# Kernel optimization log

Hardware: AMD Instinct MI355X
Metric: run time of the kernel (lower is better)

## Reference

```python
import jax, jax.numpy as jnp
import numpy as np

D1 = 4096
D2 = 4096
K = 838860  # int(D1*D2*0.05)
ALPHA = 16.0


def setup_inputs() -> dict:
    key = jax.random.key(0)
    k1, k2, k3, k4, k5 = jax.random.split(key, 5)
    x = jax.random.normal(k1, (2, 64, D1), jnp.float32)
    W_base = jax.random.normal(k2, (D2, D1), jnp.float32) * 0.02  # torch Linear weight (out, in)
    b_base = jnp.zeros((D2,), jnp.float32)
    c_re = jax.random.normal(k3, (K,), jnp.float32) * 0.02
    c_im = jax.random.normal(k4, (K,), jnp.float32) * 0.02
    # unique flat positions of the top-k frequency coefficients (stand-in for topk of |fft2(delta_W_init)|)
    mask_idx = jax.random.permutation(k5, D1 * D2)[:K].astype(jnp.int32)
    return {"x": x, "W_base": W_base, "b_base": b_base,
            "c_re": c_re, "c_im": c_im, "mask_idx": mask_idx}


def reference(x, W_base, b_base, c_re, c_im, mask_idx):
    # scatter sparse complex coefficients into dense frequency matrix
    c = (c_re + 1j * c_im).astype(jnp.complex64)
    F_flat = jnp.zeros((D1 * D2,), jnp.complex64).at[mask_idx].set(c)
    # inverse 2D FFT -> real part -> scale by alpha
    Delta_W = jnp.fft.ifft2(F_flat.reshape(D1, D2)).real.astype(jnp.float32) * ALPHA  # [D1, D2]
    # frozen base linear: h = x @ W_base.T + b
    h = jnp.einsum('bnd,fd->bnf', x, W_base) + b_base
    # LoRA-style low-frequency update
    return h + jnp.einsum('bnd,df->bnf', x, Delta_W)
```

## Files before the change

### kernel.cpp

```cpp
#include <hip/hip_runtime.h>


#define TWO_PI 6.28318530717958647692f
constexpr int NROW = 128;
constexpr float SCALE_A = 16.0f / 16777216.0f;
constexpr int NCHUNK = 256;
constexpr int KC = 4;

typedef unsigned short ushort_t;
using short8 = __attribute__((ext_vector_type(8))) short;
using f32x4  = __attribute__((ext_vector_type(4))) float;

__device__ __forceinline__ ushort_t f2bf(float f) {
  unsigned u = __float_as_uint(f);
  u = (u + 0x7FFFu + ((u >> 16) & 1u)) >> 16;
  return (ushort_t)u;
}
__device__ __forceinline__ unsigned cvtpk(float lo, float hi) {
  unsigned r;
  asm("v_cvt_pk_bf16_f32 %0, %1, %2" : "=v"(r) : "v"(lo), "v"(hi));
  return r;
}
__device__ __forceinline__ float bflo(unsigned u) { return __int_as_float((int)(u << 16)); }
__device__ __forceinline__ float bfhi(unsigned u) { return __int_as_float((int)(u & 0xffff0000u)); }
__device__ __forceinline__ void dot2(float& acc, unsigned a, unsigned b) {
  asm("v_dot2_f32_bf16 %0, %1, %2, %0" : "+v"(acc) : "v"(a), "v"(b));
}
__device__ __forceinline__ void dot2s(float& acc, unsigned a, unsigned b) {
  asm("v_dot2_f32_bf16 %0, %1, %2, %0" : "+v"(acc) : "s"(a), "v"(b));
}
__device__ __forceinline__ void gload_lds16(const void* g, void* l) {
  __builtin_amdgcn_global_load_lds(
      (const __attribute__((address_space(1))) unsigned*)g,
      (__attribute__((address_space(3))) unsigned*)l, 16, 0, 0);
}

__global__ __launch_bounds__(1024) void fused_stage1(const float* __restrict__ x,
                                                     unsigned* __restrict__ XTb,
                                                     const int* __restrict__ idx, int K,
                                                     int chunk, int* __restrict__ cnt,
                                                     ushort_t* __restrict__ xbf) {
  __shared__ __align__(16) char smem[25600];
  const int bx = blockIdx.x, tid = threadIdx.x;
  if (bx >= 512) {
    int i = (bx - 512) * 1024 + tid;
    float4 v = ((const float4*)x)[i];
    ((uint2*)xbf)[i] = make_uint2(cvtpk(v.x, v.y), cvtpk(v.z, v.w));
    return;
  }
  if (bx < 256) {
    float*    xs   = (float*)smem;
    unsigned* bp   = (unsigned*)(smem + 16384);
    float2*   w64f = (float2*)(smem + 24576);
    unsigned* wA   = (unsigned*)(smem + 25088);
    unsigned* wB   = (unsigned*)(smem + 25344);
    const int t = bx & 127, qi = bx >> 7;
    const float* xrow = x + (size_t)t * 4096;
#pragma unroll
    for (int l = 0; l < 4; ++l) xs[tid + 1024 * l] = xrow[tid + 1024 * l];
    if (tid < 64) {
      float s, c; __sincosf(TWO_PI * (float)tid * (1.0f / 64.0f), &s, &c);
      w64f[tid] = make_float2(c, s);
      wA[tid] = cvtpk(c, -s);
      wB[tid] = cvtpk(s, c);
    }
    __syncthreads();
#pragma unroll
    for (int l = 0; l < 2; ++l) {
      int o = tid + 1024 * l, m1 = o >> 5, k1l = o & 31, k1 = qi * 32 + k1l;
      float ar = 0.f, ai = 0.f;
      for (int m2 = 0; m2 < 64; ++m2) {
        float xv = xs[m1 + (m2 << 6)];
        float2 w = w64f[(m2 * k1) & 63];
        ar = fmaf(xv, w.x, ar); ai = fmaf(xv, w.y, ai);
      }
      float s, c; __sincosf((float)(m1 * k1) * (TWO_PI / 4096.0f), &s, &c);
      bp[(m1 << 5) + k1l] = cvtpk(ar * c - ai * s, ar * s + ai * c);
    }
    __syncthreads();
    {
      const int k1l = tid & 31, k2 = tid >> 5;
      const int k = qi * 32 + k1l + (k2 << 6);
      float xr = 0.f, xi = 0.f;
      for (int m1 = 0; m1 < 64; ++m1) {
        unsigned wi = (unsigned)((m1 * k2) & 63);
        unsigned bv = bp[(m1 << 5) + k1l];
        dot2(xr, wA[wi], bv);
        dot2(xi, wB[wi], bv);
      }
      XTb[(size_t)k * NROW + t] = cvtpk(xr, xi);
      if (qi == 0 && tid == 0) {
        float xr2 = 0.f, xi2 = 0.f;
        for (int m1 = 0; m1 < 64; ++m1) {
          float sgn = (m1 & 1) ? -1.f : 1.f;
          unsigned bv = bp[m1 << 5];
          xr2 = fmaf(sgn, bflo(bv), xr2);
          xi2 = fmaf(sgn, bfhi(bv), xi2);
        }
        XTb[(size_t)2048 * NROW + t] = cvtpk(xr2, xi2);
      }
    }
  } else {
    int* h = (int*)smem;
    const int c = bx - 256;
#pragma unroll
    for (int l = 0; l < 4; ++l) h[tid + 1024 * l] = 0;
    __syncthreads();
    const int j0 = c * chunk, j1 = min(j0 + chunk, K);
    for (int j = j0 + tid; j < j1; j += 1024) atomicAdd(&h[idx[j] & 4095], 1);
    __syncthreads();
#pragma unroll
    for (int l = 0; l < 4; ++l) cnt[(size_t)c * 4096 + tid + 1024 * l] = h[tid + 1024 * l];
  }
}

__global__ __launch_bounds__(256) void colscan(int* __restrict__ cnt, int* __restrict__ tot) {
  const int k2 = blockIdx.x * 256 + threadIdx.x;
  int run = 0;
  for (int c16 = 0; c16 < NCHUNK; c16 += 16) {
    int v[16];
#pragma unroll
    for (int i = 0; i < 16; ++i) v[i] = cnt[(size_t)(c16 + i) * 4096 + k2];
#pragma unroll
    for (int i = 0; i < 16; ++i) {
      cnt[(size_t)(c16 + i) * 4096 + k2] = run;
      run += v[i];
    }
  }
  tot[k2] = run;
}

__global__ __launch_bounds__(1024) void scan4096(const int* __restrict__ count,
                                                 int* __restrict__ off) {
  __shared__ int s[4096];
  int tid = threadIdx.x;
#pragma unroll
  for (int l = 0; l < 4; ++l) s[tid + 1024 * l] = count[tid + 1024 * l];
  __syncthreads();
  for (int d = 1; d < 4096; d <<= 1) {
    int v[4];
#pragma unroll
    for (int l = 0; l < 4; ++l) {
      int i = tid + 1024 * l;
      v[l] = s[i] + ((i >= d) ? s[i - d] : 0);
    }
    __syncthreads();
#pragma unroll
    for (int l = 0; l < 4; ++l) s[tid + 1024 * l] = v[l];
    __syncthreads();
  }
#pragma unroll
  for (int l = 0; l < 4; ++l) {
    int i = tid + 1024 * l;
    off[i] = s[i] - count[i];
  }
}

__global__ __launch_bounds__(1024) void scatter2(const int* __restrict__ idx,
                                                 const float* __restrict__ cre,
                                                 const float* __restrict__ cim, int K,
                                                 int chunk, const int* __restrict__ base,
                                                 const int* __restrict__ off,
                                                 uint2* __restrict__ bucket) {
  __shared__ int lbase[4096];
  __shared__ int lcur[4096];
  const int c = blockIdx.x, tid = threadIdx.x;
#pragma unroll
  for (int l = 0; l < 4; ++l) {
    int k2 = tid + 1024 * l;
    lbase[k2] = base[(size_t)c * 4096 + k2] + off[k2];
    lcur[k2] = 0;
  }
  __syncthreads();
  const int j0 = c * chunk, j1 = min(j0 + chunk, K);
  for (int j = j0 + tid; j < j1; j += 1024) {
    int p = idx[j];
    int k2 = p & 4095;
    int r = atomicAdd(&lcur[k2], 1);
    unsigned cr = f2bf(cre[j]), ci = f2bf(cim[j]);
    bucket[lbase[k2] + r] = make_uint2((unsigned)(p >> 12) | (cr << 16), ci << 16);
  }
}

#define SP_ISS1(g, u, AP, BP, XV) { \
    unsigned w0_ = (unsigned)__builtin_amdgcn_readlane((int)ec.x, (g) * 8 + (u)); \
    unsigned w1_ = (unsigned)__builtin_amdgcn_readlane((int)ec.y, (g) * 8 + (u)); \
    int k1_ = (int)(w0_ & 0xfffu); \
    unsigned cj_ = (k1_ > 2048) ? 0x8000u : 0u; \
    int r_ = (k1_ > 2048) ? 4096 - k1_ : k1_; \
    AP[u] = (w0_ >> 16) | ((((w1_ >> 16) ^ 0x8000u ^ cj_)) << 16); \
    BP[u] = (w1_ >> 16) | ((((w0_ >> 16) ^ cj_)) << 16); \
    const unsigned* p_ = XTb + (size_t)r_ * NROW; \
    asm volatile("global_load_dwordx2 %0, %1, %2" \
                 : "=v"(XV) : "v"(voff), "s"(p_) : "memory"); }
#define SP_ISS8(g, AP, BP, X) \
    SP_ISS1(g, 0, AP, BP, X##0) SP_ISS1(g, 1, AP, BP, X##1) \
    SP_ISS1(g, 2, AP, BP, X##2) SP_ISS1(g, 3, AP, BP, X##3) \
    SP_ISS1(g, 4, AP, BP, X##4) SP_ISS1(g, 5, AP, BP, X##5) \
    SP_ISS1(g, 6, AP, BP, X##6) SP_ISS1(g, 7, AP, BP, X##7)
#define SP_WAIT8(X) \
    asm volatile("s_waitcnt vmcnt(8)" \
                 : "+v"(X##0), "+v"(X##1), "+v"(X##2), "+v"(X##3), \
                   "+v"(X##4), "+v"(X##5), "+v"(X##6), "+v"(X##7) :: "memory"); \
    __builtin_amdgcn_sched_barrier(0);
#define SP_WAIT0(X) \
    asm volatile("s_waitcnt vmcnt(0)" \
                 : "+v"(X##0), "+v"(X##1), "+v"(X##2), "+v"(X##3), \
                   "+v"(X##4), "+v"(X##5), "+v"(X##6), "+v"(X##7) :: "memory"); \
    __builtin_amdgcn_sched_barrier(0);
#define SP_CMP1(u, AP, BP, XV) \
    dot2s(ar0, AP[u], XV.x); dot2s(ai0, BP[u], XV.x); \
    dot2s(ar1, AP[u], XV.y); dot2s(ai1, BP[u], XV.y);
#define SP_CMP8(AP, BP, X) \
    SP_CMP1(0, AP, BP, X##0) SP_CMP1(1, AP, BP, X##1) \
    SP_CMP1(2, AP, BP, X##2) SP_CMP1(3, AP, BP, X##3) \
    SP_CMP1(4, AP, BP, X##4) SP_CMP1(5, AP, BP, X##5) \
    SP_CMP1(6, AP, BP, X##6) SP_CMP1(7, AP, BP, X##7)

__global__ __launch_bounds__(256, 4) void fused_heavy(const uint2* __restrict__ bucket,
                                                      const int* __restrict__ off,
                                                      const int* __restrict__ count,
                                                      const unsigned* __restrict__ XTb,
                                                      unsigned* __restrict__ Yp,
                                                      const ushort_t* __restrict__ xbf,
                                                      const float* __restrict__ W,
                                                      ushort_t* __restrict__ partb) {
  __shared__ __align__(16) char smem[16384];
  const int tid = threadIdx.x;
  const int w = tid >> 6, lane = tid & 63;
  if (blockIdx.x >= 256) {
    float4* red = (float4*)smem;
    const int colsel = w >> 1, half = w & 1;
    const int k2 = (blockIdx.x - 256) * 2 + colsel;
    const int s = off[k2], n = count[k2];
    const unsigned voff = lane * 8;
    float ar0 = 0.f, ai0 = 0.f, ar1 = 0.f, ai1 = 0.f;
    for (int c = half * 64; c < n; c += 128) {
      int idx = c + lane;
      uint2 ec = (idx < n) ? bucket[s + idx] : make_uint2(0u, 0u);
      unsigned ApA[8], BpA[8], ApB[8], BpB[8];
      uint2 xa0, xa1, xa2, xa3, xa4, xa5, xa6, xa7;
      uint2 xb0, xb1, xb2, xb3, xb4, xb5, xb6, xb7;
      SP_ISS8(0, ApA, BpA, xa)
      SP_ISS8(1, ApB, BpB, xb)
      SP_WAIT8(xa) SP_CMP8(ApA, BpA, xa)
      SP_ISS8(2, ApA, BpA, xa)
      SP_WAIT8(xb) SP_CMP8(ApB, BpB, xb)
      SP_ISS8(3, ApB, BpB, xb)
      SP_WAIT8(xa) SP_CMP8(ApA, BpA, xa)
      SP_ISS8(4, ApA, BpA, xa)
      SP_WAIT8(xb) SP_CMP8(ApB, BpB, xb)
      SP_ISS8(5, ApB, BpB, xb)
      SP_WAIT8(xa) SP_CMP8(ApA, BpA, xa)
      SP_ISS8(6, ApA, BpA, xa)
      SP_WAIT8(xb) SP_CMP8(ApB, BpB, xb)
      SP_ISS8(7, ApB, BpB, xb)
      SP_WAIT8(xa) SP_CMP8(ApA, BpA, xa)
      SP_WAIT0(xb) SP_CMP8(ApB, BpB, xb)
    }
    if (half == 1) red[colsel * 64 + lane] = make_float4(ar0, ai0, ar1, ai1);
    __syncthreads();
    if (half == 0) {
      float4 o = red[colsel * 64 + lane];
      ar0 += o.x; ai0 += o.y; ar1 += o.z; ai1 += o.w;
      Yp[(size_t)(2 * lane) * 4096 + k2]     = cvtpk(ar0, ai0);
      Yp[(size_t)(2 * lane + 1) * 4096 + k2] = cvtpk(ar1, ai1);
    }
  } else {
    ushort_t* xs = (ushort_t*)smem;
    float* wsf = (float*)(smem + 8192);
    const int f0 = (blockIdx.x & 63) * 64;
    const int kc = blockIdx.x >> 6;
    f32x4 acc[2][4];
#pragma unroll
    for (int i = 0; i < 2; ++i)
#pragma unroll
      for (int j = 0; j < 4; ++j) acc[i][j] = (f32x4){0.f, 0.f, 0.f, 0.f};
    const int kbeg = kc * 1024;
    for (int st = 0; st < 32; ++st) {
      const int k0 = kbeg + st * 32;
#pragma unroll
      for (int cc = 0; cc < 2; ++cc) {
        int lb = w * 2048 + cc * 1024;
        int e = (lb >> 1) + lane * 8;
        int r = e >> 5, sl = (e >> 3) & 3;
        gload_lds16(xbf + (size_t)r * 4096 + k0 + ((sl ^ (r & 3)) << 3),
                    (char*)xs + lb);
      }
#pragma unroll
      for (int cc = 0; cc < 2; ++cc) {
        int lb = w * 2048 + cc * 1024;
        int e32 = (lb >> 2) + lane * 4;
        int r = e32 >> 5, g = (e32 >> 2) & 7, s8 = g >> 1, h = g & 1;
        gload_lds16(W + (size_t)(f0 + r) * 4096 + k0 + ((s8 ^ (r & 3)) << 3) + (h << 2),
                    (char*)wsf + lb);
      }
      __syncthreads();
      {
        int ksA = lane >> 4;
        short8 af[2], bfr[4];
#pragma unroll
        for (int mf = 0; mf < 2; ++mf) {
          int ra = w * 32 + mf * 16 + (lane & 15);
          af[mf] = *(const short8*)(&xs[ra * 32 + ((ksA ^ (ra & 3)) << 3)]);
        }
#pragma unroll
        for (int nf = 0; nf < 4; ++nf) {
          int rb = nf * 16 + (lane & 15);
          const float* bpp = &wsf[rb * 32 + ((ksA ^ (rb & 3)) << 3)];
          float4 a4 = *(const float4*)bpp;
          float4 b4 = *(const float4*)(bpp + 4);
          union { uint4 u; short8 s; } pk;
          pk.u.x = cvtpk(a4.x, a4.y);
          pk.u.y = cvtpk(a4.z, a4.w);
          pk.u.z = cvtpk(b4.x, b4.y);
          pk.u.w = cvtpk(b4.z, b4.w);
          bfr[nf] = pk.s;
        }
#pragma unroll
        for (int mf = 0; mf < 2; ++mf)
#pragma unroll
          for (int nf = 0; nf < 4; ++nf)
            acc[mf][nf] = __builtin_amdgcn_mfma_f32_16x16x32_bf16(af[mf], bfr[nf], acc[mf][nf], 0, 0, 0);
      }
      __syncthreads();
    }
    ushort_t* pb = partb + ((size_t)kc << 19);
#pragma unroll
    for (int mf = 0; mf < 2; ++mf)
#pragma unroll
      for (int nf = 0; nf < 4; ++nf)
#pragma unroll
        for (int reg = 0; reg < 4; ++reg) {
          int row = w * 32 + mf * 16 + (lane >> 4) * 4 + reg;
          int col = f0 + nf * 16 + (lane & 15);
          pb[(size_t)row * 4096 + col] = f2bf(acc[mf][nf][reg]);
        }
  }
}

__global__ __launch_bounds__(1024) void dft_rows_y(const unsigned* __restrict__ Yp,
                                                   const ushort_t* __restrict__ partb,
                                                   const float* __restrict__ bias,
                                                   float* __restrict__ out) {
  __shared__ unsigned ys[4096];
  __shared__ unsigned bp[2048];
  __shared__ unsigned wA[64], wB[64];
  const int t = blockIdx.x, qi = blockIdx.y, tid = threadIdx.x;
  const unsigned* yrow = Yp + (size_t)t * 4096;
#pragma unroll
  for (int l = 0; l < 4; ++l) ys[tid + 1024 * l] = yrow[tid + 1024 * l];
  if (tid < 64) {
    float s, c; __sincosf(TWO_PI * (float)tid * (1.0f / 64.0f), &s, &c);
    wA[tid] = cvtpk(c, -s);
    wB[tid] = cvtpk(s, c);
  }
  __syncthreads();
#pragma unroll
  for (int l = 0; l < 2; ++l) {
    int o = tid + 1024 * l, a = o >> 5, n1l = o & 31, n1 = qi * 32 + n1l;
    float ar = 0.f, ai = 0.f;
    for (int b = 0; b < 64; ++b) {
      unsigned yv = ys[a + (b << 6)];
      unsigned wi = (unsigned)((n1 * b) & 63);
      dot2(ar, wA[wi], yv);
      dot2(ai, wB[wi], yv);
    }
    float s, c; __sincosf((float)(n1 * a) * (TWO_PI / 4096.0f), &s, &c);
    bp[(a << 5) + n1l] = cvtpk(ar * c - ai * s, ar * s + ai * c);
  }
  __syncthreads();
  float* orow = out + (size_t)t * 4096;
  const int n1l = tid & 31;
  const int n1 = qi * 32 + n1l;
#pragma unroll
  for (int l = 0; l < 2; ++l) {
    int n2 = (tid >> 5) + 32 * l;
    float accv = 0.f;
    for (int a = 0; a < 64; ++a)
      dot2(accv, wA[(unsigned)((n2 * a) & 63)], bp[(a << 5) + n1l]);
    int o = n1 + (n2 << 6);
    float sum = accv * SCALE_A + bias[o];
#pragma unroll
    for (int i = 0; i < KC; ++i)
      sum += __int_as_float((int)((unsigned)partb[((size_t)i << 19) + ((size_t)t << 12) + o] << 16));
    orow[o] = sum;
  }
}

extern "C" void kernel_launch(void* const* d_in, const int* in_sizes, int n_in,
                              void* d_out, int out_size, void* d_ws, size_t ws_size,
                              hipStream_t stream) {
  const float* x   = (const float*)d_in[0];
  const float* W   = (const float*)d_in[1];
  const float* b   = (const float*)d_in[2];
  const float* cre = (const float*)d_in[3];
  const float* cim = (const float*)d_in[4];
  const int* midx  = (const int*)d_in[5];
  const int K = in_sizes[3];
  float* out = (float*)d_out;
  const int chunk = (K + NCHUNK - 1) / NCHUNK;

  char* ws = (char*)d_ws;
  unsigned* XTb   = (unsigned*)(ws);
  unsigned* Yp    = (unsigned*)(ws + ((size_t)2 << 20));
  ushort_t* xbf   = (ushort_t*)(ws + ((size_t)4 << 20));
  char* meta      = ws + ((size_t)5 << 20);
  int* tot = (int*)(meta);
  int* off = (int*)(meta + 16384);
  uint2* bucket   = (uint2*)(ws + ((size_t)5 << 20) + 262144);
  int* cnt        = (int*)(ws + ((size_t)12 << 20));
  ushort_t* partb = (ushort_t*)(ws + ((size_t)16 << 20));

  fused_stage1<<<640, 1024, 0, stream>>>(x, XTb, midx, K, chunk, cnt, xbf);
  colscan<<<16, 256, 0, stream>>>(cnt, tot);
  scan4096<<<1, 1024, 0, stream>>>(tot, off);
  scatter2<<<NCHUNK, 1024, 0, stream>>>(midx, cre, cim, K, chunk, cnt, off, bucket);
  fused_heavy<<<2304, 256, 0, stream>>>(bucket, off, tot, XTb, Yp, xbf, W, partb);
  dft_rows_y<<<dim3(NROW, 2), 1024, 0, stream>>>(Yp, partb, b, out);
}
```

Before: 106.5 us.

## Move base GEMM into the scatter kernel and split sparse column pass into own kernel

```diff
diff --git a/kernel.cpp b/kernel.cpp
--- a/kernel.cpp
+++ b/kernel.cpp
@@ -5,7 +5,7 @@
 constexpr int NROW = 128;
 constexpr float SCALE_A = 16.0f / 16777216.0f;
 constexpr int NCHUNK = 256;
-constexpr int KC = 4;
+constexpr int KC = 8;
 
 typedef unsigned short ushort_t;
 using short8 = __attribute__((ext_vector_type(8))) short;
@@ -38,7 +38,7 @@
 __global__ __launch_bounds__(1024) void fused_stage1(const float* __restrict__ x,
                                                      unsigned* __restrict__ XTb,
                                                      const int* __restrict__ idx, int K,
-                                                     int chunk, int* __restrict__ cnt,
+                                                     int chunk, ushort_t* __restrict__ cnt,
                                                      ushort_t* __restrict__ xbf) {
   __shared__ __align__(16) char smem[25600];
   const int bx = blockIdx.x, tid = threadIdx.x;
@@ -110,11 +110,13 @@
     for (int j = j0 + tid; j < j1; j += 1024) atomicAdd(&h[idx[j] & 4095], 1);
     __syncthreads();
 #pragma unroll
-    for (int l = 0; l < 4; ++l) cnt[(size_t)c * 4096 + tid + 1024 * l] = h[tid + 1024 * l];
-  }
-}
-
-__global__ __launch_bounds__(256) void colscan(int* __restrict__ cnt, int* __restrict__ tot) {
+    for (int l = 0; l < 4; ++l)
+      cnt[(size_t)c * 4096 + tid + 1024 * l] = (ushort_t)h[tid + 1024 * l];
+  }
+}
+
+__global__ __launch_bounds__(256) void colscan(ushort_t* __restrict__ cnt,
+                                               int* __restrict__ tot) {
   const int k2 = blockIdx.x * 256 + threadIdx.x;
   int run = 0;
   for (int c16 = 0; c16 < NCHUNK; c16 += 16) {
@@ -123,7 +125,7 @@
     for (int i = 0; i < 16; ++i) v[i] = cnt[(size_t)(c16 + i) * 4096 + k2];
 #pragma unroll
     for (int i = 0; i < 16; ++i) {
-      cnt[(size_t)(c16 + i) * 4096 + k2] = run;
+      cnt[(size_t)(c16 + i) * 4096 + k2] = (ushort_t)run;
       run += v[i];
     }
   }
@@ -156,29 +158,110 @@
   }
 }
 
-__global__ __launch_bounds__(1024) void scatter2(const int* __restrict__ idx,
-                                                 const float* __restrict__ cre,
-                                                 const float* __restrict__ cim, int K,
-                                                 int chunk, const int* __restrict__ base,
-                                                 const int* __restrict__ off,
-                                                 uint2* __restrict__ bucket) {
-  __shared__ int lbase[4096];
-  __shared__ int lcur[4096];
-  const int c = blockIdx.x, tid = threadIdx.x;
-#pragma unroll
-  for (int l = 0; l < 4; ++l) {
-    int k2 = tid + 1024 * l;
-    lbase[k2] = base[(size_t)c * 4096 + k2] + off[k2];
-    lcur[k2] = 0;
-  }
-  __syncthreads();
-  const int j0 = c * chunk, j1 = min(j0 + chunk, K);
-  for (int j = j0 + tid; j < j1; j += 1024) {
-    int p = idx[j];
-    int k2 = p & 4095;
-    int r = atomicAdd(&lcur[k2], 1);
-    unsigned cr = f2bf(cre[j]), ci = f2bf(cim[j]);
-    bucket[lbase[k2] + r] = make_uint2((unsigned)(p >> 12) | (cr << 16), ci << 16);
+__global__ __launch_bounds__(256) void scatter_gemm(const int* __restrict__ idx,
+                                                    const float* __restrict__ cre,
+                                                    const float* __restrict__ cim, int K,
+                                                    int chunk,
+                                                    const ushort_t* __restrict__ base,
+                                                    const int* __restrict__ off,
+                                                    uint2* __restrict__ bucket,
+                                                    const ushort_t* __restrict__ xbf,
+                                                    const float* __restrict__ W,
+                                                    ushort_t* __restrict__ partb) {
+  __shared__ __align__(16) char smem[32768];
+  const int tid = threadIdx.x;
+  if (blockIdx.x < 256) {
+    int* lbase = (int*)smem;
+    int* lcur  = (int*)(smem + 16384);
+    const int c = blockIdx.x;
+#pragma unroll
+    for (int l = 0; l < 16; ++l) {
+      int k2 = tid + 256 * l;
+      lbase[k2] = (int)base[(size_t)c * 4096 + k2] + off[k2];
+      lcur[k2] = 0;
+    }
+    __syncthreads();
+    const int j0 = c * chunk, j1 = min(j0 + chunk, K);
+    for (int j = j0 + tid; j < j1; j += 256) {
+      int p = idx[j];
+      int k2 = p & 4095;
+      int r = atomicAdd(&lcur[k2], 1);
+      unsigned cr = f2bf(cre[j]), ci = f2bf(cim[j]);
+      bucket[lbase[k2] + r] = make_uint2((unsigned)(p >> 12) | (cr << 16), ci << 16);
+    }
+  } else {
+    ushort_t* xs = (ushort_t*)smem;
+    float* wsf = (float*)(smem + 16384);
+    const int bg = blockIdx.x - 256;
+    const int f0 = (bg & 63) * 64;
+    const int kc = bg >> 6;
+    const int w = tid >> 6, lane = tid & 63;
+    f32x4 acc[2][4];
+#pragma unroll
+    for (int i = 0; i < 2; ++i)
+#pragma unroll
+      for (int j = 0; j < 4; ++j) acc[i][j] = (f32x4){0.f, 0.f, 0.f, 0.f};
+    const int kbeg = kc * 512;
+    for (int st = 0; st < 8; ++st) {
+      const int k0 = kbeg + st * 64;
+#pragma unroll
+      for (int cc = 0; cc < 4; ++cc) {
+        int lb = w * 4096 + cc * 1024;
+        int e = (lb >> 1) + lane * 8;
+        int r = e >> 6, sl = (e >> 3) & 7;
+        gload_lds16(xbf + (size_t)r * 4096 + k0 + ((sl ^ (r & 7)) << 3),
+                    (char*)xs + lb);
+      }
+#pragma unroll
+      for (int cc = 0; cc < 4; ++cc) {
+        int lb = w * 4096 + cc * 1024;
+        int e32 = (lb >> 2) + lane * 4;
+        int r = e32 >> 6, g = (e32 >> 2) & 15, s8 = g >> 1, h = g & 1;
+        gload_lds16(W + (size_t)(f0 + r) * 4096 + k0 + ((s8 ^ (r & 7)) << 3) + (h << 2),
+                    (char*)wsf + lb);
+      }
+      __syncthreads();
+#pragma unroll
+      for (int kk = 0; kk < 2; ++kk) {
+        int ksA = kk * 4 + (lane >> 4);
+        short8 af[2], bfr[4];
+#pragma unroll
+        for (int mf = 0; mf < 2; ++mf) {
+          int ra = w * 32 + mf * 16 + (lane & 15);
+          af[mf] = *(const short8*)(&xs[ra * 64 + ((ksA ^ (ra & 7)) << 3)]);
+        }
+#pragma unroll
+        for (int nf = 0; nf < 4; ++nf) {
+          int rb = nf * 16 + (lane & 15);
+          const float* bpp = &wsf[rb * 64 + ((ksA ^ (rb & 7)) << 3)];
+          float4 a4 = *(const float4*)bpp;
+          float4 b4 = *(const float4*)(bpp + 4);
+          union { uint4 u; short8 s; } pk;
+          pk.u.x = cvtpk(a4.x, a4.y);
+          pk.u.y = cvtpk(a4.z, a4.w);
+          pk.u.z = cvtpk(b4.x, b4.y);
+          pk.u.w = cvtpk(b4.z, b4.w);
+          bfr[nf] = pk.s;
+        }
+#pragma unroll
+        for (int mf = 0; mf < 2; ++mf)
+#pragma unroll
+          for (int nf = 0; nf < 4; ++nf)
+            acc[mf][nf] = __builtin_amdgcn_mfma_f32_16x16x32_bf16(af[mf], bfr[nf], acc[mf][nf], 0, 0, 0);
+      }
+      __syncthreads();
+    }
+    ushort_t* pb = partb + ((size_t)kc << 19);
+#pragma unroll
+    for (int mf = 0; mf < 2; ++mf)
+#pragma unroll
+      for (int nf = 0; nf < 4; ++nf)
+#pragma unroll
+        for (int reg = 0; reg < 4; ++reg) {
+          int row = w * 32 + mf * 16 + (lane >> 4) * 4 + reg;
+          int col = f0 + nf * 16 + (lane & 15);
+          pb[(size_t)row * 4096 + col] = f2bf(acc[mf][nf][reg]);
+        }
   }
 }
 
@@ -217,125 +300,49 @@
     SP_CMP1(4, AP, BP, X##4) SP_CMP1(5, AP, BP, X##5) \
     SP_CMP1(6, AP, BP, X##6) SP_CMP1(7, AP, BP, X##7)
 
-__global__ __launch_bounds__(256, 4) void fused_heavy(const uint2* __restrict__ bucket,
-                                                      const int* __restrict__ off,
-                                                      const int* __restrict__ count,
-                                                      const unsigned* __restrict__ XTb,
-                                                      unsigned* __restrict__ Yp,
-                                                      const ushort_t* __restrict__ xbf,
-                                                      const float* __restrict__ W,
-                                                      ushort_t* __restrict__ partb) {
-  __shared__ __align__(16) char smem[16384];
-  const int tid = threadIdx.x;
-  const int w = tid >> 6, lane = tid & 63;
-  if (blockIdx.x >= 256) {
-    float4* red = (float4*)smem;
-    const int colsel = w >> 1, half = w & 1;
-    const int k2 = (blockIdx.x - 256) * 2 + colsel;
-    const int s = off[k2], n = count[k2];
-    const unsigned voff = lane * 8;
-    float ar0 = 0.f, ai0 = 0.f, ar1 = 0.f, ai1 = 0.f;
-    for (int c = half * 64; c < n; c += 128) {
-      int idx = c + lane;
-      uint2 ec = (idx < n) ? bucket[s + idx] : make_uint2(0u, 0u);
-      unsigned ApA[8], BpA[8], ApB[8], BpB[8];
-      uint2 xa0, xa1, xa2, xa3, xa4, xa5, xa6, xa7;
-      uint2 xb0, xb1, xb2, xb3, xb4, xb5, xb6, xb7;
-      SP_ISS8(0, ApA, BpA, xa)
-      SP_ISS8(1, ApB, BpB, xb)
-      SP_WAIT8(xa) SP_CMP8(ApA, BpA, xa)
-      SP_ISS8(2, ApA, BpA, xa)
-      SP_WAIT8(xb) SP_CMP8(ApB, BpB, xb)
-      SP_ISS8(3, ApB, BpB, xb)
-      SP_WAIT8(xa) SP_CMP8(ApA, BpA, xa)
-      SP_ISS8(4, ApA, BpA, xa)
-      SP_WAIT8(xb) SP_CMP8(ApB, BpB, xb)
-      SP_ISS8(5, ApB, BpB, xb)
-      SP_WAIT8(xa) SP_CMP8(ApA, BpA, xa)
-      SP_ISS8(6, ApA, BpA, xa)
-      SP_WAIT8(xb) SP_CMP8(ApB, BpB, xb)
-      SP_ISS8(7, ApB, BpB, xb)
-      SP_WAIT8(xa) SP_CMP8(ApA, BpA, xa)
-      SP_WAIT0(xb) SP_CMP8(ApB, BpB, xb)
-    }
-    if (half == 1) red[colsel * 64 + lane] = make_float4(ar0, ai0, ar1, ai1);
-    __syncthreads();
-    if (half == 0) {
-      float4 o = red[colsel * 64 + lane];
-      ar0 += o.x; ai0 += o.y; ar1 += o.z; ai1 += o.w;
-      Yp[(size_t)(2 * lane) * 4096 + k2]     = cvtpk(ar0, ai0);
-      Yp[(size_t)(2 * lane + 1) * 4096 + k2] = cvtpk(ar1, ai1);
-    }
-  } else {
-    ushort_t* xs = (ushort_t*)smem;
-    float* wsf = (float*)(smem + 8192);
-    const int f0 = (blockIdx.x & 63) * 64;
-    const int kc = blockIdx.x >> 6;
-    f32x4 acc[2][4];
-#pragma unroll
-    for (int i = 0; i < 2; ++i)
-#pragma unroll
-      for (int j = 0; j < 4; ++j) acc[i][j] = (f32x4){0.f, 0.f, 0.f, 0.f};
-    const int kbeg = kc * 1024;
-    for (int st = 0; st < 32; ++st) {
-      const int k0 = kbeg + st * 32;
-#pragma unroll
-      for (int cc = 0; cc < 2; ++cc) {
-        int lb = w * 2048 + cc * 1024;
-        int e = (lb >> 1) + lane * 8;
-        int r = e >> 5, sl = (e >> 3) & 3;
-        gload_lds16(xbf + (size_t)r * 4096 + k0 + ((sl ^ (r & 3)) << 3),
-                    (char*)xs + lb);
-      }
-#pragma unroll
-      for (int cc = 0; cc < 2; ++cc) {
-        int lb = w * 2048 + cc * 1024;
-        int e32 = (lb >> 2) + lane * 4;
-        int r = e32 >> 5, g = (e32 >> 2) & 7, s8 = g >> 1, h = g & 1;
-        gload_lds16(W + (size_t)(f0 + r) * 4096 + k0 + ((s8 ^ (r & 3)) << 3) + (h << 2),
-                    (char*)wsf + lb);
-      }
-      __syncthreads();
-      {
-        int ksA = lane >> 4;
-        short8 af[2], bfr[4];
-#pragma unroll
-        for (int mf = 0; mf < 2; ++mf) {
-          int ra = w * 32 + mf * 16 + (lane & 15);
-          af[mf] = *(const short8*)(&xs[ra * 32 + ((ksA ^ (ra & 3)) << 3)]);
-        }
-#pragma unroll
-        for (int nf = 0; nf < 4; ++nf) {
-          int rb = nf * 16 + (lane & 15);
-          const float* bpp = &wsf[rb * 32 + ((ksA ^ (rb & 3)) << 3)];
-          float4 a4 = *(const float4*)bpp;
-          float4 b4 = *(const float4*)(bpp + 4);
-          union { uint4 u; short8 s; } pk;
-          pk.u.x = cvtpk(a4.x, a4.y);
-          pk.u.y = cvtpk(a4.z, a4.w);
-          pk.u.z = cvtpk(b4.x, b4.y);
-          pk.u.w = cvtpk(b4.z, b4.w);
-          bfr[nf] = pk.s;
-        }
-#pragma unroll
-        for (int mf = 0; mf < 2; ++mf)
-#pragma unroll
-          for (int nf = 0; nf < 4; ++nf)
-            acc[mf][nf] = __builtin_amdgcn_mfma_f32_16x16x32_bf16(af[mf], bfr[nf], acc[mf][nf], 0, 0, 0);
-      }
-      __syncthreads();
-    }
-    ushort_t* pb = partb + ((size_t)kc << 19);
-#pragma unroll
-    for (int mf = 0; mf < 2; ++mf)
-#pragma unroll
-      for (int nf = 0; nf < 4; ++nf)
-#pragma unroll
-        for (int reg = 0; reg < 4; ++reg) {
-          int row = w * 32 + mf * 16 + (lane >> 4) * 4 + reg;
-          int col = f0 + nf * 16 + (lane & 15);
-          pb[(size_t)row * 4096 + col] = f2bf(acc[mf][nf][reg]);
-        }
+__global__ __launch_bounds__(256, 4) void spmm_col(const uint2* __restrict__ bucket,
+                                                   const int* __restrict__ off,
+                                                   const int* __restrict__ count,
+                                                   const unsigned* __restrict__ XTb,
+                                                   unsigned* __restrict__ Yp) {
+  __shared__ float4 red[2][64];
+  const int lane = threadIdx.x & 63;
+  const int wid = threadIdx.x >> 6;
+  const int colsel = wid >> 1, half = wid & 1;
+  const int k2 = blockIdx.x * 2 + colsel;
+  const int s = off[k2], n = count[k2];
+  const unsigned voff = lane * 8;
+  float ar0 = 0.f, ai0 = 0.f, ar1 = 0.f, ai1 = 0.f;
+  for (int c = half * 64; c < n; c += 128) {
+    int idx = c + lane;
+    uint2 ec = (idx < n) ? bucket[s + idx] : make_uint2(0u, 0u);
+    unsigned ApA[8], BpA[8], ApB[8], BpB[8];
+    uint2 xa0, xa1, xa2, xa3, xa4, xa5, xa6, xa7;
+    uint2 xb0, xb1, xb2, xb3, xb4, xb5, xb6, xb7;
+    SP_ISS8(0, ApA, BpA, xa)
+    SP_ISS8(1, ApB, BpB, xb)
+    SP_WAIT8(xa) SP_CMP8(ApA, BpA, xa)
+    SP_ISS8(2, ApA, BpA, xa)
+    SP_WAIT8(xb) SP_CMP8(ApB, BpB, xb)
+    SP_ISS8(3, ApB, BpB, xb)
+    SP_WAIT8(xa) SP_CMP8(ApA, BpA, xa)
+    SP_ISS8(4, ApA, BpA, xa)
+    SP_WAIT8(xb) SP_CMP8(ApB, BpB, xb)
+    SP_ISS8(5, ApB, BpB, xb)
+    SP_WAIT8(xa) SP_CMP8(ApA, BpA, xa)
+    SP_ISS8(6, ApA, BpA, xa)
+    SP_WAIT8(xb) SP_CMP8(ApB, BpB, xb)
+    SP_ISS8(7, ApB, BpB, xb)
+    SP_WAIT8(xa) SP_CMP8(ApA, BpA, xa)
+    SP_WAIT0(xb) SP_CMP8(ApB, BpB, xb)
+  }
+  if (half == 1) red[colsel][lane] = make_float4(ar0, ai0, ar1, ai1);
+  __syncthreads();
+  if (half == 0) {
+    float4 o = red[colsel][lane];
+    ar0 += o.x; ai0 += o.y; ar1 += o.z; ai1 += o.w;
+    Yp[(size_t)(2 * lane) * 4096 + k2]     = cvtpk(ar0, ai0);
+    Yp[(size_t)(2 * lane + 1) * 4096 + k2] = cvtpk(ar1, ai1);
   }
 }
 
@@ -409,13 +416,14 @@
   int* tot = (int*)(meta);
   int* off = (int*)(meta + 16384);
   uint2* bucket   = (uint2*)(ws + ((size_t)5 << 20) + 262144);
-  int* cnt        = (int*)(ws + ((size_t)12 << 20));
-  ushort_t* partb = (ushort_t*)(ws + ((size_t)16 << 20));
+  ushort_t* cnt   = (ushort_t*)(ws + ((size_t)12 << 20));
+  ushort_t* partb = (ushort_t*)(ws + ((size_t)14 << 20));
 
   fused_stage1<<<640, 1024, 0, stream>>>(x, XTb, midx, K, chunk, cnt, xbf);
   colscan<<<16, 256, 0, stream>>>(cnt, tot);
   scan4096<<<1, 1024, 0, stream>>>(tot, off);
-  scatter2<<<NCHUNK, 1024, 0, stream>>>(midx, cre, cim, K, chunk, cnt, off, bucket);
-  fused_heavy<<<2304, 256, 0, stream>>>(bucket, off, tot, XTb, Yp, xbf, W, partb);
+  scatter_gemm<<<768, 256, 0, stream>>>(midx, cre, cim, K, chunk, cnt, off, bucket,
+                                        xbf, W, partb);
+  spmm_col<<<2048, 256, 0, stream>>>(bucket, off, tot, XTb, Yp);
   dft_rows_y<<<dim3(NROW, 2), 1024, 0, stream>>>(Yp, partb, b, out);
 }
```

Measured after the change: 111.7 us. 4.8% more time.
